# Optimization experiments

Measured on AMD Instinct MI355X. Metric: run time of the kernel, lower is better.

Reference implementation:

```python
import jax, jax.numpy as jnp
import numpy as np

B, N, D, H, HD, C = 2, 2048, 2048, 16, 128, 128  # batch, seq, embed, heads, head_dim, chunk
EPS = 1e-6


def setup_inputs() -> dict:
    key = jax.random.key(0)
    ks = jax.random.split(key, 9)
    s = 0.02
    x = jax.random.normal(ks[0], (B, N, D), jnp.float32)
    # per-head negative log decay (lambda = exp(log_decay) in (0,1))
    log_decay = -jax.random.uniform(ks[1], (H,), jnp.float32, minval=0.01, maxval=1.0)
    Wq = jax.random.normal(ks[2], (D, D), jnp.float32) * s
    Wk = jax.random.normal(ks[3], (D, D), jnp.float32) * s
    Wv = jax.random.normal(ks[4], (D, D), jnp.float32) * s
    Wo = jax.random.normal(ks[5], (D, D), jnp.float32) * s
    Wg1 = jax.random.normal(ks[6], (D, HD), jnp.float32) * s
    Wg2 = jax.random.normal(ks[7], (HD, D), jnp.float32) * s
    norm_w = jnp.ones((D,), jnp.float32)
    return dict(x=x, log_decay=log_decay, Wq=Wq, Wk=Wk, Wv=Wv, Wo=Wo,
                Wg1=Wg1, Wg2=Wg2, norm_w=norm_w)


def _lasd(q, k, v, ld):
    # causal linear attention with per-head scalar log-decay, chunked scan.
    # q,k,v: [B,N,H,HD]; ld: [H] (negative). Recurrence: S_t = exp(ld)*S_{t-1} + k_t v_t^T; o_t = q_t @ S_t
    nc = N // C
    to_chunks = lambda t: t.reshape(B, nc, C, H, HD).transpose(1, 0, 3, 2, 4)  # [nc,B,H,C,HD]
    qc, kc, vc = map(to_chunks, (q, k, v))
    i = jnp.arange(C, dtype=jnp.float32)
    diff = i[:, None] - i[None, :]                     # [C,C]
    Dm = jnp.exp(jnp.where(diff >= 0, ld[:, None, None] * diff, -jnp.inf))  # [H,C,C]
    dq = jnp.exp(ld[:, None] * (i + 1.0))              # [H,C] decay applied to q vs chunk-start state
    dk = jnp.exp(ld[:, None] * (C - 1.0 - i))          # [H,C] decay applied to k for state update
    dS = jnp.exp(ld * C)                               # [H]   chunk-level state decay

    def step(S, qkv):
        qb, kb, vb = qkv                               # [B,H,C,HD]
        attn = jnp.einsum('bhid,bhjd->bhij', qb, kb) * Dm
        o = jnp.einsum('bhij,bhje->bhie', attn, vb)
        o = o + jnp.einsum('bhid,bhde->bhie', qb * dq[None, :, :, None], S)
        S = S * dS[None, :, None, None] + jnp.einsum('bhjd,bhje->bhde', kb * dk[None, :, :, None], vb)
        return S, o

    S0 = jnp.zeros((B, H, HD, HD), jnp.float32)
    _, o = jax.lax.scan(step, S0, (qc, kc, vc))        # [nc,B,H,C,HD]
    return o.transpose(1, 0, 3, 2, 4).reshape(B, N, H, HD)


def reference(x, log_decay, Wq, Wk, Wv, Wo, Wg1, Wg2, norm_w):
    silu = jax.nn.silu
    q = silu(x @ Wq).reshape(B, N, H, HD)
    k = silu(x @ Wk).reshape(B, N, H, HD)
    v = silu(x @ Wv).reshape(B, N, H, HD)
    o = _lasd(q, k, v, log_decay).reshape(B, N, D)
    gate = jax.nn.sigmoid((x @ Wg1) @ Wg2)             # two stacked linears, no nonlinearity between
    o = o * gate
    o = o * jax.lax.rsqrt(jnp.mean(o * o, axis=-1, keepdims=True) + EPS) * norm_w  # rmsnorm
    return o @ Wo
```

## Files before the change

### kernel.cpp

```cpp
#include <hip/hip_runtime.h>
#include <hip/hip_bf16.h>
#include <cstdint>
#include <cstddef>

#define B_   2
#define N_   2048
#define D_   2048
#define H_   16
#define HD_  128
#define C_   128
#define NC_  16
#define M_   4096
#define QKVG_ 8192

typedef __attribute__((ext_vector_type(8))) short bf16x8;
typedef __attribute__((ext_vector_type(4))) float f32x4;

__device__ __forceinline__ uint16_t f2bf(float f){
  __hip_bfloat16 h = __float2bfloat16(f);
  return *reinterpret_cast<uint16_t*>(&h);
}
__device__ __forceinline__ float bf2f(uint16_t u){
  union { uint32_t i; float f; } v; v.i = ((uint32_t)u) << 16; return v.f;
}

__device__ __forceinline__ void async16(const uint16_t* g, uint16_t* l){
  __builtin_amdgcn_global_load_lds(
      (const __attribute__((address_space(1))) void*)g,
      (__attribute__((address_space(3))) void*)l, 16, 0, 0);
}

__device__ __forceinline__ int swz(int row, int c){
  return row*128 + ((((c >> 3) ^ row) & 15) << 3) + (c & 7);
}

__device__ __forceinline__ int swz32(int row, int kc8){
  return row*32 + (((kc8 ^ row) & 3) << 3);
}

__global__ __launch_bounds__(256) void cast_kernel(
    const float* __restrict__ x, uint16_t* __restrict__ y)
{
  int i = (blockIdx.x*256 + threadIdx.x)*4;
  float4 f = *(const float4*)(x + i);
  ushort4 u;
  u.x = f2bf(f.x); u.y = f2bf(f.y); u.z = f2bf(f.z); u.w = f2bf(f.w);
  *(ushort4*)(y + i) = u;
}

__global__ __launch_bounds__(256) void transpose_cast(
    const float* __restrict__ W, uint16_t* __restrict__ Wt, int R, int Cc)
{
  __shared__ uint16_t tile[32][33];
  const int tx = threadIdx.x & 31;
  const int ty = threadIdx.x >> 5;
  const int r0 = blockIdx.y*32, c0 = blockIdx.x*32;
  #pragma unroll
  for (int rr = 0; rr < 4; ++rr){
    int r = ty + rr*8;
    tile[r][tx] = f2bf(W[(size_t)(r0 + r)*Cc + c0 + tx]);
  }
  __syncthreads();
  #pragma unroll
  for (int rr = 0; rr < 4; ++rr){
    int r = ty + rr*8;
    Wt[(size_t)(c0 + r)*R + r0 + tx] = tile[tx][r];
  }
}

template<int ACT, int OUTBF>
__global__ __launch_bounds__(256)
void gemm_bt(const uint16_t* __restrict__ A, const uint16_t* __restrict__ Bt,
             void* __restrict__ Cout, int M, int Ncols, int K)
{
  __shared__ __align__(16) uint16_t As[128*32];
  __shared__ __align__(16) uint16_t Bs[128*32];
  const int t    = threadIdx.x;
  const int lane = t & 63, wave = t >> 6;
  const int wm = wave >> 1, wn = wave & 1;
  const int row0 = wm*64, col0 = wn*64;
  const int lr = lane & 15, kq = lane >> 4;

  const uint16_t* Ap = A  + (size_t)(blockIdx.y*128)*K;
  const uint16_t* Bp = Bt + (size_t)(blockIdx.x*128)*K;

  const f32x4 zero = {0.f, 0.f, 0.f, 0.f};
  f32x4 acc[4][4];
  #pragma unroll
  for (int i = 0; i < 4; ++i)
    #pragma unroll
    for (int j = 0; j < 4; ++j) acc[i][j] = zero;

  const int r0c = t >> 2;
  const int kc0 = ((t & 3) ^ (r0c & 3)) * 8;

  for (int k0 = 0; k0 < K; k0 += 32){
    async16(Ap + (size_t)r0c*K      + k0 + kc0, As + t*8);
    async16(Ap + (size_t)(r0c+64)*K + k0 + kc0, As + (t+256)*8);
    async16(Bp + (size_t)r0c*K      + k0 + kc0, Bs + t*8);
    async16(Bp + (size_t)(r0c+64)*K + k0 + kc0, Bs + (t+256)*8);
    __syncthreads();
    bf16x8 af[4], bfr[4];
    #pragma unroll
    for (int i = 0; i < 4; ++i)
      af[i]  = *(const bf16x8*)(As + swz32(row0 + i*16 + lr, kq));
    #pragma unroll
    for (int j = 0; j < 4; ++j)
      bfr[j] = *(const bf16x8*)(Bs + swz32(col0 + j*16 + lr, kq));
    #pragma unroll
    for (int i = 0; i < 4; ++i)
      #pragma unroll
      for (int j = 0; j < 4; ++j)
        acc[i][j] = __builtin_amdgcn_mfma_f32_16x16x32_bf16(af[i], bfr[j], acc[i][j], 0, 0, 0);
    __syncthreads();
  }

  const int mode = (ACT == 3) ? ((blockIdx.x < 48) ? 1 : 2) : ACT;
  const int orow0 = blockIdx.y*128 + row0 + kq*4;
  const int ocol0 = blockIdx.x*128 + col0 + lr;
  #pragma unroll
  for (int i = 0; i < 4; ++i){
    #pragma unroll
    for (int j = 0; j < 4; ++j){
      #pragma unroll
      for (int r = 0; r < 4; ++r){
        float v = acc[i][j][r];
        if (mode == 1)      v = v / (1.f + __expf(-v));
        else if (mode == 2) v = 1.f / (1.f + __expf(-v));
        size_t off = (size_t)(orow0 + i*16 + r)*Ncols + (ocol0 + j*16);
        if (OUTBF) ((uint16_t*)Cout)[off] = f2bf(v);
        else       ((float*)Cout)[off]    = v;
      }
    }
  }
}

__global__ __launch_bounds__(256)
void chunk_state_kernel(const uint16_t* __restrict__ qkvg,
                        const float* __restrict__ log_decay, uint16_t* __restrict__ MsumT)
{
  __shared__ __align__(16) uint16_t vT[128*128];
  __shared__ __align__(16) uint16_t kT[128*128];
  const int h = blockIdx.x, b = blockIdx.y, ic = blockIdx.z;
  const int t    = threadIdx.x;
  const int lane = t & 63, wave = t >> 6;
  const int wm = wave >> 1, wn = wave & 1;
  const int e0 = wm*64, d0 = wn*64;
  const int lr = lane & 15, kq = lane >> 4;
  const float ld = log_decay[h];
  const size_t rowbase = (size_t)b*N_ + (size_t)ic*C_;
  const uint16_t* kb = qkvg + (size_t)D_;
  const uint16_t* vb = qkvg + (size_t)2*D_;

  #pragma unroll 4
  for (int it = 0; it < 64; ++it){
    int idx = t + it*256;
    int j = idx >> 7, e = idx & 127;
    uint16_t vv = vb[(rowbase + j)*QKVG_ + h*HD_ + e];
    float kf = bf2f(kb[(rowbase + j)*QKVG_ + h*HD_ + e]) * __expf(ld * (float)(C_ - 1 - j));
    vT[swz(e, j)] = vv;
    kT[swz(e, j)] = f2bf(kf);
  }
  __syncthreads();

  const f32x4 zero = {0.f, 0.f, 0.f, 0.f};
  f32x4 acc[4][4];
  #pragma unroll
  for (int i = 0; i < 4; ++i)
    #pragma unroll
    for (int j = 0; j < 4; ++j) acc[i][j] = zero;

  #pragma unroll
  for (int kt = 0; kt < 4; ++kt){
    bf16x8 af[4], bfr[4];
    #pragma unroll
    for (int i = 0; i < 4; ++i)
      af[i]  = *(const bf16x8*)(vT + swz(e0 + i*16 + lr, kt*32 + kq*8));
    #pragma unroll
    for (int j = 0; j < 4; ++j)
      bfr[j] = *(const bf16x8*)(kT + swz(d0 + j*16 + lr, kt*32 + kq*8));
    #pragma unroll
    for (int i = 0; i < 4; ++i)
      #pragma unroll
      for (int j = 0; j < 4; ++j)
        acc[i][j] = __builtin_amdgcn_mfma_f32_16x16x32_bf16(af[i], bfr[j], acc[i][j], 0, 0, 0);
  }

  uint16_t* Mout = MsumT + (((size_t)ic*B_ + b)*H_ + h)*(size_t)(HD_*HD_);
  #pragma unroll
  for (int i = 0; i < 4; ++i)
    #pragma unroll
    for (int j = 0; j < 4; ++j)
      #pragma unroll
      for (int r = 0; r < 4; ++r)
        Mout[(size_t)(e0 + i*16 + kq*4 + r)*HD_ + d0 + j*16 + lr] = f2bf(acc[i][j][r]);
}

__global__ __launch_bounds__(256)
void scan_kernel(const uint16_t* __restrict__ MsumT, const float* __restrict__ log_decay,
                 uint16_t* __restrict__ StT)
{
  const int h = blockIdx.x, b = blockIdx.y;
  const float ld = log_decay[h];
  const float dS = __expf(ld * (float)C_);
  const int base_e = blockIdx.z*2048;
  float cur[8];
  #pragma unroll
  for (int r = 0; r < 8; ++r) cur[r] = 0.f;
  for (int i = 0; i < NC_; ++i){
    const size_t base = (((size_t)i*B_ + b)*H_ + h)*(size_t)(HD_*HD_) + base_e;
    #pragma unroll
    for (int r = 0; r < 8; ++r){
      int idx = threadIdx.x + r*256;
      StT[base + idx] = f2bf(cur[r]);
      cur[r] = cur[r]*dS + bf2f(MsumT[base + idx]);
    }
  }
}

__global__ __launch_bounds__(256)
void attn_kernel(const uint16_t* __restrict__ qkvg, const uint16_t* __restrict__ StT,
                 const float* __restrict__ log_decay, float* __restrict__ o_attn)
{
  __shared__ __align__(16) uint16_t Ps[128*128];
  __shared__ __align__(16) uint16_t vT[128*128];
  const int h = blockIdx.x, b = blockIdx.y, ic = blockIdx.z;
  const int t    = threadIdx.x;
  const int lane = t & 63, wave = t >> 6;
  const int wm = wave >> 1, wn = wave & 1;
  const int row0 = wm*64, col0 = wn*64;
  const int lr = lane & 15, kq = lane >> 4;
  const float ld = log_decay[h];
  const size_t rowbase = (size_t)b*N_ + (size_t)ic*C_;
  const uint16_t* qb = qkvg;
  const uint16_t* kb = qkvg + (size_t)D_;
  const uint16_t* vb = qkvg + (size_t)2*D_;

  #pragma unroll 4
  for (int it = 0; it < 64; ++it){
    int idx = t + it*256;
    int j = idx >> 7, e = idx & 127;
    vT[swz(e, j)] = vb[(rowbase + j)*QKVG_ + h*HD_ + e];
  }

  const f32x4 zero = {0.f, 0.f, 0.f, 0.f};
  f32x4 acc[4][4];
  #pragma unroll
  for (int i = 0; i < 4; ++i)
    #pragma unroll
    for (int j = 0; j < 4; ++j) acc[i][j] = zero;

  #pragma unroll
  for (int kt = 0; kt < 4; ++kt){
    bf16x8 af[4], bfr[4];
    #pragma unroll
    for (int i = 0; i < 4; ++i)
      af[i]  = *(const bf16x8*)(qb + (rowbase + row0 + i*16 + lr)*QKVG_ + h*HD_ + kt*32 + kq*8);
    #pragma unroll
    for (int j = 0; j < 4; ++j)
      bfr[j] = *(const bf16x8*)(kb + (rowbase + col0 + j*16 + lr)*QKVG_ + h*HD_ + kt*32 + kq*8);
    #pragma unroll
    for (int i = 0; i < 4; ++i)
      #pragma unroll
      for (int j = 0; j < 4; ++j)
        acc[i][j] = __builtin_amdgcn_mfma_f32_16x16x32_bf16(af[i], bfr[j], acc[i][j], 0, 0, 0);
  }
  #pragma unroll
  for (int i = 0; i < 4; ++i)
    #pragma unroll
    for (int j = 0; j < 4; ++j)
      #pragma unroll
      for (int r = 0; r < 4; ++r){
        int row = row0 + i*16 + kq*4 + r;
        int col = col0 + j*16 + lr;
        int dlt = row - col;
        float f = (dlt >= 0) ? __expf(ld * (float)dlt) : 0.f;
        Ps[swz(row, col)] = f2bf(acc[i][j][r] * f);
      }

  #pragma unroll
  for (int i = 0; i < 4; ++i)
    #pragma unroll
    for (int j = 0; j < 4; ++j) acc[i][j] = zero;
  const uint16_t* Sb = StT + (((size_t)ic*B_ + b)*H_ + h)*(size_t)(HD_*HD_);
  #pragma unroll
  for (int kt = 0; kt < 4; ++kt){
    bf16x8 af[4], bfr[4];
    #pragma unroll
    for (int i = 0; i < 4; ++i)
      af[i]  = *(const bf16x8*)(qb + (rowbase + row0 + i*16 + lr)*QKVG_ + h*HD_ + kt*32 + kq*8);
    #pragma unroll
    for (int j = 0; j < 4; ++j)
      bfr[j] = *(const bf16x8*)(Sb + (size_t)(col0 + j*16 + lr)*HD_ + kt*32 + kq*8);
    #pragma unroll
    for (int i = 0; i < 4; ++i)
      #pragma unroll
      for (int j = 0; j < 4; ++j)
        acc[i][j] = __builtin_amdgcn_mfma_f32_16x16x32_bf16(af[i], bfr[j], acc[i][j], 0, 0, 0);
  }
  #pragma unroll
  for (int i = 0; i < 4; ++i)
    #pragma unroll
    for (int r = 0; r < 4; ++r){
      float dqv = __expf(ld * (float)(row0 + i*16 + kq*4 + r + 1));
      #pragma unroll
      for (int j = 0; j < 4; ++j) acc[i][j][r] *= dqv;
    }

  __syncthreads();

  #pragma unroll
  for (int kt = 0; kt < 4; ++kt){
    bf16x8 af[4], bfr[4];
    #pragma unroll
    for (int i = 0; i < 4; ++i)
      af[i]  = *(const bf16x8*)(Ps + swz(row0 + i*16 + lr, kt*32 + kq*8));
    #pragma unroll
    for (int j = 0; j < 4; ++j)
      bfr[j] = *(const bf16x8*)(vT + swz(col0 + j*16 + lr, kt*32 + kq*8));
    #pragma unroll
    for (int i = 0; i < 4; ++i)
      #pragma unroll
      for (int j = 0; j < 4; ++j)
        acc[i][j] = __builtin_amdgcn_mfma_f32_16x16x32_bf16(af[i], bfr[j], acc[i][j], 0, 0, 0);
  }

  #pragma unroll
  for (int i = 0; i < 4; ++i)
    #pragma unroll
    for (int j = 0; j < 4; ++j)
      #pragma unroll
      for (int r = 0; r < 4; ++r){
        int row = row0 + i*16 + kq*4 + r;
        int col = col0 + j*16 + lr;
        o_attn[(rowbase + row)*D_ + h*HD_ + col] = acc[i][j][r];
      }
}

__global__ __launch_bounds__(256)
void gate_norm_kernel(const float* __restrict__ o_attn, const uint16_t* __restrict__ qkvg,
                      const float* __restrict__ norm_w, uint16_t* __restrict__ on)
{
  const int row = blockIdx.x;
  const int t = threadIdx.x;
  const int c1 = t*4, c2 = 1024 + t*4;
  const float*    orow = o_attn + (size_t)row*D_;
  const uint16_t* grow = qkvg + (size_t)row*QKVG_ + 3*D_;
  float4  o1 = *(const float4*)(orow + c1);
  float4  o2 = *(const float4*)(orow + c2);
  ushort4 g1 = *(const ushort4*)(grow + c1);
  ushort4 g2 = *(const ushort4*)(grow + c2);
  float v[8];
  v[0] = o1.x*bf2f(g1.x); v[1] = o1.y*bf2f(g1.y); v[2] = o1.z*bf2f(g1.z); v[3] = o1.w*bf2f(g1.w);
  v[4] = o2.x*bf2f(g2.x); v[5] = o2.y*bf2f(g2.y); v[6] = o2.z*bf2f(g2.z); v[7] = o2.w*bf2f(g2.w);
  float s = 0.f;
  #pragma unroll
  for (int k = 0; k < 8; ++k) s += v[k]*v[k];
  #pragma unroll
  for (int off = 32; off > 0; off >>= 1) s += __shfl_down(s, off);
  __shared__ float red[4];
  if ((t & 63) == 0) red[t >> 6] = s;
  __syncthreads();
  float total = red[0] + red[1] + red[2] + red[3];
  float scale = rsqrtf(total * (1.f/(float)D_) + 1e-6f);
  float4 w1 = *(const float4*)(norm_w + c1);
  float4 w2 = *(const float4*)(norm_w + c2);
  ushort4 b1, b2;
  b1.x = f2bf(v[0]*scale*w1.x); b1.y = f2bf(v[1]*scale*w1.y);
  b1.z = f2bf(v[2]*scale*w1.z); b1.w = f2bf(v[3]*scale*w1.w);
  b2.x = f2bf(v[4]*scale*w2.x); b2.y = f2bf(v[5]*scale*w2.y);
  b2.z = f2bf(v[6]*scale*w2.z); b2.w = f2bf(v[7]*scale*w2.w);
  *(ushort4*)(on + (size_t)row*D_ + c1) = b1;
  *(ushort4*)(on + (size_t)row*D_ + c2) = b2;
}

extern "C" void kernel_launch(void* const* d_in, const int* in_sizes, int n_in,
                              void* d_out, int out_size, void* d_ws, size_t ws_size,
                              hipStream_t stream) {
  const float* x         = (const float*)d_in[0];
  const float* log_decay = (const float*)d_in[1];
  const float* Wq        = (const float*)d_in[2];
  const float* Wk        = (const float*)d_in[3];
  const float* Wv        = (const float*)d_in[4];
  const float* Wo        = (const float*)d_in[5];
  const float* Wg1       = (const float*)d_in[6];
  const float* Wg2       = (const float*)d_in[7];
  const float* norm_w    = (const float*)d_in[8];
  float* out = (float*)d_out;

  uint8_t* p = (uint8_t*)d_ws;
  uint16_t* xb    = (uint16_t*)p; p += (size_t)M_*D_*2;
  uint16_t* WT    = (uint16_t*)p; p += (size_t)QKVG_*D_*2;
  uint16_t* WoT   = (uint16_t*)p; p += (size_t)D_*D_*2;
  uint16_t* Wg1b  = (uint16_t*)p; p += (size_t)D_*HD_*2;
  uint16_t* Wg2T  = (uint16_t*)p; p += (size_t)D_*HD_*2;
  uint16_t* qkvg  = (uint16_t*)p; p += (size_t)M_*QKVG_*2;
  uint16_t* MsumT = (uint16_t*)p; p += (size_t)NC_*B_*H_*HD_*HD_*2;
  uint16_t* StT   = (uint16_t*)p; p += (size_t)NC_*B_*H_*HD_*HD_*2;
  float*    o_att = (float*)WT;
  uint16_t* on    = xb;

  cast_kernel<<<(M_*D_)/1024, 256, 0, stream>>>(x, xb);
  cast_kernel<<<(D_*HD_)/1024, 256, 0, stream>>>(Wg1, Wg1b);
  transpose_cast<<<dim3(D_/32, D_/32), 256, 0, stream>>>(Wq, WT,               D_, D_);
  transpose_cast<<<dim3(D_/32, D_/32), 256, 0, stream>>>(Wk, WT + 2048*2048,   D_, D_);
  transpose_cast<<<dim3(D_/32, D_/32), 256, 0, stream>>>(Wv, WT + 2*2048*2048, D_, D_);
  transpose_cast<<<dim3(D_/32, D_/32), 256, 0, stream>>>(Wo, WoT,              D_, D_);
  transpose_cast<<<dim3(D_/32, HD_/32), 256, 0, stream>>>(Wg2, Wg2T, HD_, D_);

  gemm_bt<0,1><<<dim3(D_/128, D_/128), 256, 0, stream>>>(Wg2T, Wg1b, WT + (size_t)3*2048*2048, D_, D_, HD_);

  gemm_bt<3,1><<<dim3(QKVG_/128, M_/128), 256, 0, stream>>>(xb, WT, qkvg, M_, QKVG_, D_);

  chunk_state_kernel<<<dim3(H_, B_, NC_), 256, 0, stream>>>(qkvg, log_decay, MsumT);
  scan_kernel<<<dim3(H_, B_, 8), 256, 0, stream>>>(MsumT, log_decay, StT);
  attn_kernel<<<dim3(H_, B_, NC_), 256, 0, stream>>>(qkvg, StT, log_decay, o_att);

  gate_norm_kernel<<<M_, 256, 0, stream>>>(o_att, qkvg, norm_w, on);
  gemm_bt<0,0><<<dim3(D_/128, M_/128), 256, 0, stream>>>(on, WoT, out, M_, D_, D_);
}
```

Baseline: 467.4 us.

## Rework GEMMs with 32x32 MFMA and K=64 tiles, fuse weight prep, split-K output GEMM

The GEMM kernel now uses 32x32x16 bf16 MFMA instructions with 64-wide K tiles and an 8-way XOR swizzle, which halves the number of barriers per K and cuts LDS fragment reads. The five transpose/cast launches and the Wg1 cast are merged into a single prep_weights launch. The output projection GEMM is split along K into two partial fp32 buffers that a separate add kernel sums, doubling its block count to fill more CUs. The cost is extra memory traffic for the partial sums and one more launch.

```diff
diff --git a/kernel.cpp b/kernel.cpp
--- a/kernel.cpp
+++ b/kernel.cpp
@@ -15,6 +15,7 @@
 
 typedef __attribute__((ext_vector_type(8))) short bf16x8;
 typedef __attribute__((ext_vector_type(4))) float f32x4;
+typedef __attribute__((ext_vector_type(16))) float f32x16;
 
 __device__ __forceinline__ uint16_t f2bf(float f){
   __hip_bfloat16 h = __float2bfloat16(f);
@@ -32,10 +33,6 @@
 
 __device__ __forceinline__ int swz(int row, int c){
   return row*128 + ((((c >> 3) ^ row) & 15) << 3) + (c & 7);
-}
-
-__device__ __forceinline__ int swz32(int row, int kc8){
-  return row*32 + (((kc8 ^ row) & 3) << 3);
 }
 
 __global__ __launch_bounds__(256) void cast_kernel(
@@ -48,91 +45,139 @@
   *(ushort4*)(y + i) = u;
 }
 
-__global__ __launch_bounds__(256) void transpose_cast(
-    const float* __restrict__ W, uint16_t* __restrict__ Wt, int R, int Cc)
-{
-  __shared__ uint16_t tile[32][33];
+__global__ __launch_bounds__(256)
+void prep_weights(const float* __restrict__ Wq, const float* __restrict__ Wk,
+                  const float* __restrict__ Wv, const float* __restrict__ Wo,
+                  const float* __restrict__ Wg2, const float* __restrict__ Wg1,
+                  uint16_t* __restrict__ WT, uint16_t* __restrict__ WoT,
+                  uint16_t* __restrict__ Wg2T, uint16_t* __restrict__ Wg1b)
+{
+  const int z = blockIdx.z;
   const int tx = threadIdx.x & 31;
   const int ty = threadIdx.x >> 5;
+  __shared__ uint16_t tile[32][33];
+
+  if (z == 5){
+    if (blockIdx.x >= 4) return;
+    const int r0 = blockIdx.y*32, c0 = blockIdx.x*32;
+    #pragma unroll
+    for (int rr = 0; rr < 4; ++rr){
+      int r = r0 + ty + rr*8;
+      Wg1b[(size_t)r*HD_ + c0 + tx] = f2bf(Wg1[(size_t)r*HD_ + c0 + tx]);
+    }
+    return;
+  }
+
+  const float* src; uint16_t* dst; int R, Cc;
+  if (z < 3)      { src = (z==0)?Wq:(z==1)?Wk:Wv; dst = WT + (size_t)z*D_*D_; R = D_; Cc = D_; }
+  else if (z == 3){ src = Wo;  dst = WoT;  R = D_;  Cc = D_; }
+  else            { if (blockIdx.y >= 4) return;
+                    src = Wg2; dst = Wg2T; R = HD_; Cc = D_; }
+
   const int r0 = blockIdx.y*32, c0 = blockIdx.x*32;
   #pragma unroll
   for (int rr = 0; rr < 4; ++rr){
     int r = ty + rr*8;
-    tile[r][tx] = f2bf(W[(size_t)(r0 + r)*Cc + c0 + tx]);
+    tile[r][tx] = f2bf(src[(size_t)(r0 + r)*Cc + c0 + tx]);
   }
   __syncthreads();
   #pragma unroll
   for (int rr = 0; rr < 4; ++rr){
     int r = ty + rr*8;
-    Wt[(size_t)(c0 + r)*R + r0 + tx] = tile[tx][r];
+    dst[(size_t)(c0 + r)*R + r0 + tx] = tile[tx][r];
   }
 }
 
 template<int ACT, int OUTBF>
 __global__ __launch_bounds__(256)
-void gemm_bt(const uint16_t* __restrict__ A, const uint16_t* __restrict__ Bt,
-             void* __restrict__ Cout, int M, int Ncols, int K)
-{
-  __shared__ __align__(16) uint16_t As[128*32];
-  __shared__ __align__(16) uint16_t Bs[128*32];
+void gemm_bt2(const uint16_t* __restrict__ A, const uint16_t* __restrict__ Bt,
+              void* __restrict__ Cout, int M, int Ncols, int K, int klen)
+{
+  __shared__ __align__(16) uint16_t As[128*64];
+  __shared__ __align__(16) uint16_t Bs[128*64];
   const int t    = threadIdx.x;
   const int lane = t & 63, wave = t >> 6;
   const int wm = wave >> 1, wn = wave & 1;
   const int row0 = wm*64, col0 = wn*64;
-  const int lr = lane & 15, kq = lane >> 4;
+  const int lm = lane & 31, lh = lane >> 5;
 
   const uint16_t* Ap = A  + (size_t)(blockIdx.y*128)*K;
   const uint16_t* Bp = Bt + (size_t)(blockIdx.x*128)*K;
-
-  const f32x4 zero = {0.f, 0.f, 0.f, 0.f};
-  f32x4 acc[4][4];
-  #pragma unroll
-  for (int i = 0; i < 4; ++i)
-    #pragma unroll
-    for (int j = 0; j < 4; ++j) acc[i][j] = zero;
-
-  const int r0c = t >> 2;
-  const int kc0 = ((t & 3) ^ (r0c & 3)) * 8;
-
-  for (int k0 = 0; k0 < K; k0 += 32){
-    async16(Ap + (size_t)r0c*K      + k0 + kc0, As + t*8);
-    async16(Ap + (size_t)(r0c+64)*K + k0 + kc0, As + (t+256)*8);
-    async16(Bp + (size_t)r0c*K      + k0 + kc0, Bs + t*8);
-    async16(Bp + (size_t)(r0c+64)*K + k0 + kc0, Bs + (t+256)*8);
+  const int kbeg = blockIdx.z * klen;
+
+  f32x16 acc[2][2];
+  #pragma unroll
+  for (int i = 0; i < 2; ++i)
+    #pragma unroll
+    for (int j = 0; j < 2; ++j)
+      #pragma unroll
+      for (int r = 0; r < 16; ++r) acc[i][j][r] = 0.f;
+
+  const int srow = t >> 3;
+  const int gch  = (t & 7) ^ (srow & 7);
+  const size_t aoff0 = (size_t)srow*K + gch*8;
+
+  for (int k0 = kbeg; k0 < kbeg + klen; k0 += 64){
+    #pragma unroll
+    for (int c = 0; c < 4; ++c){
+      async16(Ap + (size_t)(c*32)*K + aoff0 + k0, As + c*2048 + t*8);
+      async16(Bp + (size_t)(c*32)*K + aoff0 + k0, Bs + c*2048 + t*8);
+    }
     __syncthreads();
-    bf16x8 af[4], bfr[4];
-    #pragma unroll
-    for (int i = 0; i < 4; ++i)
-      af[i]  = *(const bf16x8*)(As + swz32(row0 + i*16 + lr, kq));
-    #pragma unroll
-    for (int j = 0; j < 4; ++j)
-      bfr[j] = *(const bf16x8*)(Bs + swz32(col0 + j*16 + lr, kq));
-    #pragma unroll
-    for (int i = 0; i < 4; ++i)
-      #pragma unroll
-      for (int j = 0; j < 4; ++j)
-        acc[i][j] = __builtin_amdgcn_mfma_f32_16x16x32_bf16(af[i], bfr[j], acc[i][j], 0, 0, 0);
+    #pragma unroll
+    for (int kh = 0; kh < 4; ++kh){
+      bf16x8 af[2], bfr[2];
+      const int ch = kh*2 + lh;
+      #pragma unroll
+      for (int i = 0; i < 2; ++i){
+        int r = row0 + i*32 + lm;
+        af[i] = *(const bf16x8*)(As + r*64 + ((ch ^ (r & 7)) << 3));
+      }
+      #pragma unroll
+      for (int j = 0; j < 2; ++j){
+        int r = col0 + j*32 + lm;
+        bfr[j] = *(const bf16x8*)(Bs + r*64 + ((ch ^ (r & 7)) << 3));
+      }
+      #pragma unroll
+      for (int i = 0; i < 2; ++i)
+        #pragma unroll
+        for (int j = 0; j < 2; ++j)
+          acc[i][j] = __builtin_amdgcn_mfma_f32_32x32x16_bf16(af[i], bfr[j], acc[i][j], 0, 0, 0);
+    }
     __syncthreads();
   }
 
   const int mode = (ACT == 3) ? ((blockIdx.x < 48) ? 1 : 2) : ACT;
-  const int orow0 = blockIdx.y*128 + row0 + kq*4;
-  const int ocol0 = blockIdx.x*128 + col0 + lr;
-  #pragma unroll
-  for (int i = 0; i < 4; ++i){
-    #pragma unroll
-    for (int j = 0; j < 4; ++j){
-      #pragma unroll
-      for (int r = 0; r < 4; ++r){
+  uint16_t* outb = (uint16_t*)Cout;
+  float*    outf = (float*)Cout + (OUTBF ? 0 : (size_t)blockIdx.z*M*Ncols);
+  #pragma unroll
+  for (int i = 0; i < 2; ++i){
+    #pragma unroll
+    for (int j = 0; j < 2; ++j){
+      #pragma unroll
+      for (int r = 0; r < 16; ++r){
+        int row = blockIdx.y*128 + row0 + i*32 + (r & 3) + 8*(r >> 2) + 4*lh;
+        int col = blockIdx.x*128 + col0 + j*32 + lm;
         float v = acc[i][j][r];
         if (mode == 1)      v = v / (1.f + __expf(-v));
         else if (mode == 2) v = 1.f / (1.f + __expf(-v));
-        size_t off = (size_t)(orow0 + i*16 + r)*Ncols + (ocol0 + j*16);
-        if (OUTBF) ((uint16_t*)Cout)[off] = f2bf(v);
-        else       ((float*)Cout)[off]    = v;
+        size_t off = (size_t)row*Ncols + col;
+        if (OUTBF) outb[off] = f2bf(v);
+        else       outf[off] = v;
       }
     }
   }
+}
+
+__global__ __launch_bounds__(256)
+void add_kernel(const float* __restrict__ p0, const float* __restrict__ p1,
+                float* __restrict__ out)
+{
+  int i = (blockIdx.x*256 + threadIdx.x)*4;
+  float4 a = *(const float4*)(p0 + i);
+  float4 b = *(const float4*)(p1 + i);
+  float4 o; o.x = a.x+b.x; o.y = a.y+b.y; o.z = a.z+b.z; o.w = a.w+b.w;
+  *(float4*)(out + i) = o;
 }
 
 __global__ __launch_bounds__(256)
@@ -399,23 +444,24 @@
   uint16_t* StT   = (uint16_t*)p; p += (size_t)NC_*B_*H_*HD_*HD_*2;
   float*    o_att = (float*)WT;
   uint16_t* on    = xb;
+  float*    part  = (float*)qkvg;
 
   cast_kernel<<<(M_*D_)/1024, 256, 0, stream>>>(x, xb);
-  cast_kernel<<<(D_*HD_)/1024, 256, 0, stream>>>(Wg1, Wg1b);
-  transpose_cast<<<dim3(D_/32, D_/32), 256, 0, stream>>>(Wq, WT,               D_, D_);
-  transpose_cast<<<dim3(D_/32, D_/32), 256, 0, stream>>>(Wk, WT + 2048*2048,   D_, D_);
-  transpose_cast<<<dim3(D_/32, D_/32), 256, 0, stream>>>(Wv, WT + 2*2048*2048, D_, D_);
-  transpose_cast<<<dim3(D_/32, D_/32), 256, 0, stream>>>(Wo, WoT,              D_, D_);
-  transpose_cast<<<dim3(D_/32, HD_/32), 256, 0, stream>>>(Wg2, Wg2T, HD_, D_);
-
-  gemm_bt<0,1><<<dim3(D_/128, D_/128), 256, 0, stream>>>(Wg2T, Wg1b, WT + (size_t)3*2048*2048, D_, D_, HD_);
-
-  gemm_bt<3,1><<<dim3(QKVG_/128, M_/128), 256, 0, stream>>>(xb, WT, qkvg, M_, QKVG_, D_);
+  prep_weights<<<dim3(64, 64, 6), 256, 0, stream>>>(Wq, Wk, Wv, Wo, Wg2, Wg1,
+                                                    WT, WoT, Wg2T, Wg1b);
+
+  gemm_bt2<0,1><<<dim3(D_/128, D_/128, 1), 256, 0, stream>>>(
+      Wg2T, Wg1b, WT + (size_t)3*D_*D_, D_, D_, HD_, HD_);
+
+  gemm_bt2<3,1><<<dim3(QKVG_/128, M_/128, 1), 256, 0, stream>>>(
+      xb, WT, qkvg, M_, QKVG_, D_, D_);
 
   chunk_state_kernel<<<dim3(H_, B_, NC_), 256, 0, stream>>>(qkvg, log_decay, MsumT);
   scan_kernel<<<dim3(H_, B_, 8), 256, 0, stream>>>(MsumT, log_decay, StT);
   attn_kernel<<<dim3(H_, B_, NC_), 256, 0, stream>>>(qkvg, StT, log_decay, o_att);
 
   gate_norm_kernel<<<M_, 256, 0, stream>>>(o_att, qkvg, norm_w, on);
-  gemm_bt<0,0><<<dim3(D_/128, M_/128), 256, 0, stream>>>(on, WoT, out, M_, D_, D_);
-}
+  gemm_bt2<0,0><<<dim3(D_/128, M_/128, 2), 256, 0, stream>>>(
+      on, WoT, part, M_, D_, D_, D_/2);
+  add_kernel<<<(M_*D_)/1024, 256, 0, stream>>>(part, part + (size_t)M_*D_, out);
+}
```

Result: faster. 449.9 us (-3.7%).
